# Optimization experiments

Measured on AMD Instinct MI355X. Metric: run time of the kernel, lower is better.

## Reference

```python
import jax, jax.numpy as jnp
import numpy as np

ALIGN_CORNERS = True
APPLY_SMOOTHSTEP = True

SIZES = [(32, 32, 32), (64, 64, 64), (128, 128, 128), (256, 256, 256)]
FEAT_DIMS = [4, 4, 4, 4]
N_POINTS = 1048576  # 2**20 sample points (e.g. 8192 rays x 128 samples)


def setup_inputs() -> dict:
    key = jax.random.key(0)
    ks = jax.random.split(key, 1 + len(SIZES))
    # grid_sample-style coords in [-1, 1], layout [1, 1, 1, N, 3] (x, y, z)
    grid = jax.random.uniform(ks[0], (1, 1, 1, N_POINTS, 3), dtype=jnp.float32) * 2.0 - 1.0
    inp = {"grid": grid}
    for i, (size, c) in enumerate(zip(SIZES, FEAT_DIMS)):
        # original init: (rand(1,C,1,1,1)*2-1).repeat over spatial; use randn volumes for a
        # non-degenerate baseline (same shapes/math path)
        inp[f"vol{i}"] = jax.random.normal(ks[1 + i], (1, c, *size), dtype=jnp.float32)
    return inp


def _smooth_sample(vol, grid_pts):
    """Trilinear sample with border padding, align_corners=True, smoothstep weights.

    vol: [C, D, H, W]; grid_pts: [P, 3] with (x, y, z) in [-1, 1].
    Returns [C, P].
    """
    C, D, H, W = vol.shape
    # unnormalize (align_corners=True): [-1,1] -> [0, dim-1]; border padding via clip
    x = jnp.clip((grid_pts[:, 0] + 1.0) * 0.5 * (W - 1), 0.0, W - 1)
    y = jnp.clip((grid_pts[:, 1] + 1.0) * 0.5 * (H - 1), 0.0, H - 1)
    z = jnp.clip((grid_pts[:, 2] + 1.0) * 0.5 * (D - 1), 0.0, D - 1)

    x0 = jnp.floor(x); y0 = jnp.floor(y); z0 = jnp.floor(z)
    tx = x - x0; ty = y - y0; tz = z - z0
    if APPLY_SMOOTHSTEP:
        tx = tx * tx * (3.0 - 2.0 * tx)
        ty = ty * ty * (3.0 - 2.0 * ty)
        tz = tz * tz * (3.0 - 2.0 * tz)

    x0i = x0.astype(jnp.int32); x1i = jnp.minimum(x0i + 1, W - 1)
    y0i = y0.astype(jnp.int32); y1i = jnp.minimum(y0i + 1, H - 1)
    z0i = z0.astype(jnp.int32); z1i = jnp.minimum(z0i + 1, D - 1)

    # 8 corner gathers -> [C, P]
    c000 = vol[:, z0i, y0i, x0i]; c001 = vol[:, z0i, y0i, x1i]
    c010 = vol[:, z0i, y1i, x0i]; c011 = vol[:, z0i, y1i, x1i]
    c100 = vol[:, z1i, y0i, x0i]; c101 = vol[:, z1i, y0i, x1i]
    c110 = vol[:, z1i, y1i, x0i]; c111 = vol[:, z1i, y1i, x1i]

    c00 = c000 + (c001 - c000) * tx
    c01 = c010 + (c011 - c010) * tx
    c10 = c100 + (c101 - c100) * tx
    c11 = c110 + (c111 - c110) * tx
    c0 = c00 + (c01 - c00) * ty
    c1 = c10 + (c11 - c10) * ty
    return c0 + (c1 - c0) * tz


def reference(grid, vol0, vol1, vol2, vol3):
    # grid: [1, 1, 1, N, 3] -> [N, 3]
    pts = grid.reshape(-1, 3)
    n = pts.shape[0]
    out = []
    for vol in (vol0, vol1, vol2, vol3):
        feat = _smooth_sample(vol[0], pts)            # [C, N]
        out.append(feat.reshape(1, -1, 1, 1, n))      # grid_sample output layout
    return jnp.concatenate(out, axis=1)               # [1, sum(C), 1, 1, N]
```

## Files before the change

### kernel.cpp

```cpp
#include <hip/hip_runtime.h>

#define NPTS 1048576
#define NB 32
#define NBINS (NB * NB * NB)

typedef float v4f __attribute__((ext_vector_type(4)));

__device__ __forceinline__ void nt_store4(const float4& f, float4* p) {
    __builtin_nontemporal_store(*(const v4f*)&f, (v4f*)p);
}


__device__ __forceinline__ float4 lerp4(const float4 a, const float4 b, const float t) {
    return make_float4(a.x + (b.x - a.x) * t,
                       a.y + (b.y - a.y) * t,
                       a.z + (b.z - a.z) * t,
                       a.w + (b.w - a.w) * t);
}

struct CoordW { float tx, ty, tz; int b00, b01, b10, b11, x0, x1; };

template<int D>
__device__ __forceinline__ CoordW mkcoord(float gx, float gy, float gz) {
    CoordW c;
    float x = fminf(fmaxf((gx + 1.0f) * (0.5f * (float)(D - 1)), 0.0f), (float)(D - 1));
    float y = fminf(fmaxf((gy + 1.0f) * (0.5f * (float)(D - 1)), 0.0f), (float)(D - 1));
    float z = fminf(fmaxf((gz + 1.0f) * (0.5f * (float)(D - 1)), 0.0f), (float)(D - 1));
    float xf = floorf(x), yf = floorf(y), zf = floorf(z);
    float tx = x - xf, ty = y - yf, tz = z - zf;
    c.tx = tx * tx * (3.0f - 2.0f * tx);
    c.ty = ty * ty * (3.0f - 2.0f * ty);
    c.tz = tz * tz * (3.0f - 2.0f * tz);
    int x0 = (int)xf, y0 = (int)yf, z0 = (int)zf;
    int y1 = min(y0 + 1, D - 1), z1 = min(z0 + 1, D - 1);
    c.x0 = x0;
    c.x1 = min(x0 + 1, D - 1);
    c.b00 = (z0 * D + y0) * D;
    c.b01 = (z0 * D + y1) * D;
    c.b10 = (z1 * D + y0) * D;
    c.b11 = (z1 * D + y1) * D;
    return c;
}

__device__ __forceinline__ float4 reduce8(const float4* q, const CoordW& c) {
    float4 c00 = lerp4(q[0], q[1], c.tx);
    float4 c01 = lerp4(q[2], q[3], c.tx);
    float4 c10 = lerp4(q[4], q[5], c.tx);
    float4 c11 = lerp4(q[6], q[7], c.tx);
    float4 c0 = lerp4(c00, c01, c.ty);
    float4 c1 = lerp4(c10, c11, c.ty);
    return lerp4(c0, c1, c.tz);
}


#define DHW0 (32 * 32 * 32)
#define DHW1 (64 * 64 * 64)
#define DHW2 (128 * 128 * 128)

__global__ __launch_bounds__(256) void xpose_all_kernel(
    const float* __restrict__ v0, const float* __restrict__ v1, const float* __restrict__ v2,
    float4* __restrict__ w0, float4* __restrict__ w1, float4* __restrict__ w2)
{
    constexpr int B2 = DHW2 / 256, B1 = DHW1 / 256;
    int b = blockIdx.x;
    int t = threadIdx.x;
    if (b < B2) {
        int v = b * 256 + t;
        w2[v] = make_float4(v2[v], v2[v + DHW2], v2[v + 2 * DHW2], v2[v + 3 * DHW2]);
    } else if (b < B2 + B1) {
        int v = (b - B2) * 256 + t;
        w1[v] = make_float4(v1[v], v1[v + DHW1], v1[v + 2 * DHW1], v1[v + 3 * DHW1]);
    } else {
        int v = (b - B2 - B1) * 256 + t;
        w0[v] = make_float4(v0[v], v0[v + DHW0], v0[v + 2 * DHW0], v0[v + 3 * DHW0]);
    }
}


__device__ __forceinline__ int bin_of(float gx, float gy, float gz) {
    float ux = fminf(fmaxf((gx + 1.0f) * 0.5f, 0.0f), 1.0f);
    float uy = fminf(fmaxf((gy + 1.0f) * 0.5f, 0.0f), 1.0f);
    float uz = fminf(fmaxf((gz + 1.0f) * 0.5f, 0.0f), 1.0f);
    int bx = min((int)(ux * (float)NB), NB - 1);
    int by = min((int)(uy * (float)NB), NB - 1);
    int bz = min((int)(uz * (float)NB), NB - 1);
    return (bz * NB + by) * NB + bx;
}

__global__ __launch_bounds__(256) void bin_hist_kernel(const float* __restrict__ grid,
                                                       unsigned* __restrict__ hist) {
    int p = blockIdx.x * blockDim.x + threadIdx.x;
    float gx = grid[3 * p + 0];
    float gy = grid[3 * p + 1];
    float gz = grid[3 * p + 2];
    atomicAdd(&hist[bin_of(gx, gy, gz)], 1u);
}

__global__ __launch_bounds__(1024) void scan_kernel(const unsigned* __restrict__ hist,
                                                    unsigned* __restrict__ offsets) {
    __shared__ unsigned partial[1024];
    const int t = threadIdx.x;
    const int base = t * 32;
    unsigned sum = 0;
#pragma unroll
    for (int i = 0; i < 32; ++i) sum += hist[base + i];
    partial[t] = sum;
    __syncthreads();
    for (int off = 1; off < 1024; off <<= 1) {
        unsigned v = (t >= off) ? partial[t - off] : 0u;
        __syncthreads();
        partial[t] += v;
        __syncthreads();
    }
    unsigned run = partial[t] - sum;
#pragma unroll
    for (int i = 0; i < 32; ++i) {
        offsets[base + i] = run;
        run += hist[base + i];
    }
}

__global__ __launch_bounds__(256) void scatter_kernel(const float* __restrict__ grid,
                                                      unsigned* __restrict__ offsets,
                                                      float4* __restrict__ sorted,
                                                      int* __restrict__ inv) {
    int p = blockIdx.x * blockDim.x + threadIdx.x;
    float gx = grid[3 * p + 0];
    float gy = grid[3 * p + 1];
    float gz = grid[3 * p + 2];
    int b = bin_of(gx, gy, gz);
    unsigned pos = atomicAdd(&offsets[b], 1u);
    sorted[pos] = make_float4(gx, gy, gz, __int_as_float(p));
    inv[p] = (int)pos;
}


__global__ __launch_bounds__(256, 4) void gather_sorted_kernel(
    const float4* __restrict__ sorted,
    const float4* __restrict__ w0, const float4* __restrict__ w1,
    const float4* __restrict__ w2, const float* __restrict__ v3,
    float4* __restrict__ wsout)
{
    int bid = blockIdx.x;
    int sb = (bid & 7) * (int)(gridDim.x >> 3) + (bid >> 3);
    int s = sb * 256 + (int)threadIdx.x;
    float4 gp = sorted[s];
    float gx = gp.x, gy = gp.y, gz = gp.z;

    CoordW c0 = mkcoord<32>(gx, gy, gz);
    CoordW c1 = mkcoord<64>(gx, gy, gz);
    CoordW c2 = mkcoord<128>(gx, gy, gz);
    CoordW c3 = mkcoord<256>(gx, gy, gz);

    float4 qa[8], qb[8], qc[8];
    qa[0] = w0[c0.b00 + c0.x0]; qa[1] = w0[c0.b00 + c0.x1];
    qa[2] = w0[c0.b01 + c0.x0]; qa[3] = w0[c0.b01 + c0.x1];
    qa[4] = w0[c0.b10 + c0.x0]; qa[5] = w0[c0.b10 + c0.x1];
    qa[6] = w0[c0.b11 + c0.x0]; qa[7] = w0[c0.b11 + c0.x1];

    qb[0] = w1[c1.b00 + c1.x0]; qb[1] = w1[c1.b00 + c1.x1];
    qb[2] = w1[c1.b01 + c1.x0]; qb[3] = w1[c1.b01 + c1.x1];
    qb[4] = w1[c1.b10 + c1.x0]; qb[5] = w1[c1.b10 + c1.x1];
    qb[6] = w1[c1.b11 + c1.x0]; qb[7] = w1[c1.b11 + c1.x1];

    qc[0] = w2[c2.b00 + c2.x0]; qc[1] = w2[c2.b00 + c2.x1];
    qc[2] = w2[c2.b01 + c2.x0]; qc[3] = w2[c2.b01 + c2.x1];
    qc[4] = w2[c2.b10 + c2.x0]; qc[5] = w2[c2.b10 + c2.x1];
    qc[6] = w2[c2.b11 + c2.x0]; qc[7] = w2[c2.b11 + c2.x1];

    const int xm = min(c3.x0, 254);
    const bool edge = (c3.x0 == 255);
    float2 qd[16];
#pragma unroll
    for (int ch = 0; ch < 4; ++ch) {
        const float* __restrict__ vc = v3 + (size_t)ch * (256 * 256 * 256);
        qd[ch * 4 + 0] = *(const float2*)(vc + c3.b00 + xm);
        qd[ch * 4 + 1] = *(const float2*)(vc + c3.b01 + xm);
        qd[ch * 4 + 2] = *(const float2*)(vc + c3.b10 + xm);
        qd[ch * 4 + 3] = *(const float2*)(vc + c3.b11 + xm);
    }

    float4 f0 = reduce8(qa, c0);
    float4 f1 = reduce8(qb, c1);
    float4 f2 = reduce8(qc, c2);

    float r3[4];
#pragma unroll
    for (int ch = 0; ch < 4; ++ch) {
        float v00a = edge ? qd[ch * 4 + 0].y : qd[ch * 4 + 0].x, v00b = qd[ch * 4 + 0].y;
        float v01a = edge ? qd[ch * 4 + 1].y : qd[ch * 4 + 1].x, v01b = qd[ch * 4 + 1].y;
        float v10a = edge ? qd[ch * 4 + 2].y : qd[ch * 4 + 2].x, v10b = qd[ch * 4 + 2].y;
        float v11a = edge ? qd[ch * 4 + 3].y : qd[ch * 4 + 3].x, v11b = qd[ch * 4 + 3].y;
        float c00 = v00a + (v00b - v00a) * c3.tx;
        float c01 = v01a + (v01b - v01a) * c3.tx;
        float c10 = v10a + (v10b - v10a) * c3.tx;
        float c11 = v11a + (v11b - v11a) * c3.tx;
        float e0 = c00 + (c01 - c00) * c3.ty;
        float e1 = c10 + (c11 - c10) * c3.ty;
        r3[ch] = e0 + (e1 - e0) * c3.tz;
    }
    float4 f3 = make_float4(r3[0], r3[1], r3[2], r3[3]);

    float4* w = wsout + (size_t)s * 4;
    nt_store4(f0, w + 0);
    nt_store4(f1, w + 1);
    nt_store4(f2, w + 2);
    nt_store4(f3, w + 3);
}


__device__ __forceinline__ void permute_one(const float4* __restrict__ wsout,
                                            const int* __restrict__ inv,
                                            float* __restrict__ out, int p) {
    int s = inv[p];
    const float4* w = wsout + (size_t)s * 4;
    float4 f0 = w[0], f1 = w[1], f2 = w[2], f3 = w[3];
    __builtin_nontemporal_store(f0.x, &out[ 0 * NPTS + p]);
    __builtin_nontemporal_store(f0.y, &out[ 1 * NPTS + p]);
    __builtin_nontemporal_store(f0.z, &out[ 2 * NPTS + p]);
    __builtin_nontemporal_store(f0.w, &out[ 3 * NPTS + p]);
    __builtin_nontemporal_store(f1.x, &out[ 4 * NPTS + p]);
    __builtin_nontemporal_store(f1.y, &out[ 5 * NPTS + p]);
    __builtin_nontemporal_store(f1.z, &out[ 6 * NPTS + p]);
    __builtin_nontemporal_store(f1.w, &out[ 7 * NPTS + p]);
    __builtin_nontemporal_store(f2.x, &out[ 8 * NPTS + p]);
    __builtin_nontemporal_store(f2.y, &out[ 9 * NPTS + p]);
    __builtin_nontemporal_store(f2.z, &out[10 * NPTS + p]);
    __builtin_nontemporal_store(f2.w, &out[11 * NPTS + p]);
    __builtin_nontemporal_store(f3.x, &out[12 * NPTS + p]);
    __builtin_nontemporal_store(f3.y, &out[13 * NPTS + p]);
    __builtin_nontemporal_store(f3.z, &out[14 * NPTS + p]);
    __builtin_nontemporal_store(f3.w, &out[15 * NPTS + p]);
}

__global__ __launch_bounds__(256) void permute_kernel(const float4* __restrict__ wsout,
                                                      const int* __restrict__ inv,
                                                      float* __restrict__ out) {
    int p = blockIdx.x * blockDim.x + threadIdx.x;
    permute_one(wsout, inv, out, p);
    permute_one(wsout, inv, out, p + NPTS / 2);
}


template<int D>
__device__ __forceinline__ float4 sample_inter(const float4* __restrict__ v,
                                               float gx, float gy, float gz) {
    CoordW c = mkcoord<D>(gx, gy, gz);
    float4 q[8];
    q[0] = v[c.b00 + c.x0]; q[1] = v[c.b00 + c.x1];
    q[2] = v[c.b01 + c.x0]; q[3] = v[c.b01 + c.x1];
    q[4] = v[c.b10 + c.x0]; q[5] = v[c.b10 + c.x1];
    q[6] = v[c.b11 + c.x0]; q[7] = v[c.b11 + c.x1];
    return reduce8(q, c);
}

template<int D>
__device__ __forceinline__ float4 sample_direct(const float* __restrict__ v,
                                                float gx, float gy, float gz) {
    CoordW c = mkcoord<D>(gx, gy, gz);
    float r[4];
#pragma unroll
    for (int ch = 0; ch < 4; ++ch) {
        const float* __restrict__ vc = v + (size_t)ch * (D * D * D);
        float c000 = vc[c.b00 + c.x0], c001 = vc[c.b00 + c.x1];
        float c010 = vc[c.b01 + c.x0], c011 = vc[c.b01 + c.x1];
        float c100 = vc[c.b10 + c.x0], c101 = vc[c.b10 + c.x1];
        float c110 = vc[c.b11 + c.x0], c111 = vc[c.b11 + c.x1];
        float c00 = c000 + (c001 - c000) * c.tx;
        float c01 = c010 + (c011 - c010) * c.tx;
        float c10 = c100 + (c101 - c100) * c.tx;
        float c11 = c110 + (c111 - c110) * c.tx;
        float e0 = c00 + (c01 - c00) * c.ty;
        float e1 = c10 + (c11 - c10) * c.ty;
        r[ch] = e0 + (e1 - e0) * c.tz;
    }
    return make_float4(r[0], r[1], r[2], r[3]);
}

__global__ __launch_bounds__(256) void mg_direct_kernel(
    const float* __restrict__ grid,
    const float* __restrict__ v0, const float* __restrict__ v1,
    const float* __restrict__ v2, const float* __restrict__ v3,
    float* __restrict__ out)
{
    int p = blockIdx.x * blockDim.x + threadIdx.x;
    float gx = grid[3 * p + 0];
    float gy = grid[3 * p + 1];
    float gz = grid[3 * p + 2];
    float4 f0 = sample_direct<32>(v0, gx, gy, gz);
    float4 f1 = sample_direct<64>(v1, gx, gy, gz);
    float4 f2 = sample_direct<128>(v2, gx, gy, gz);
    float4 f3 = sample_direct<256>(v3, gx, gy, gz);
    out[ 0 * NPTS + p] = f0.x; out[ 1 * NPTS + p] = f0.y;
    out[ 2 * NPTS + p] = f0.z; out[ 3 * NPTS + p] = f0.w;
    out[ 4 * NPTS + p] = f1.x; out[ 5 * NPTS + p] = f1.y;
    out[ 6 * NPTS + p] = f1.z; out[ 7 * NPTS + p] = f1.w;
    out[ 8 * NPTS + p] = f2.x; out[ 9 * NPTS + p] = f2.y;
    out[10 * NPTS + p] = f2.z; out[11 * NPTS + p] = f2.w;
    out[12 * NPTS + p] = f3.x; out[13 * NPTS + p] = f3.y;
    out[14 * NPTS + p] = f3.z; out[15 * NPTS + p] = f3.w;
}

__global__ __launch_bounds__(256) void mg_inter_kernel(
    const float* __restrict__ grid,
    const float4* __restrict__ w0, const float4* __restrict__ w1,
    const float4* __restrict__ w2, const float* __restrict__ v3,
    float* __restrict__ out)
{
    int p = blockIdx.x * blockDim.x + threadIdx.x;
    float gx = grid[3 * p + 0];
    float gy = grid[3 * p + 1];
    float gz = grid[3 * p + 2];
    float4 f0 = sample_inter<32>(w0, gx, gy, gz);
    float4 f1 = sample_inter<64>(w1, gx, gy, gz);
    float4 f2 = sample_inter<128>(w2, gx, gy, gz);
    float4 f3 = sample_direct<256>(v3, gx, gy, gz);
    out[ 0 * NPTS + p] = f0.x; out[ 1 * NPTS + p] = f0.y;
    out[ 2 * NPTS + p] = f0.z; out[ 3 * NPTS + p] = f0.w;
    out[ 4 * NPTS + p] = f1.x; out[ 5 * NPTS + p] = f1.y;
    out[ 6 * NPTS + p] = f1.z; out[ 7 * NPTS + p] = f1.w;
    out[ 8 * NPTS + p] = f2.x; out[ 9 * NPTS + p] = f2.y;
    out[10 * NPTS + p] = f2.z; out[11 * NPTS + p] = f2.w;
    out[12 * NPTS + p] = f3.x; out[13 * NPTS + p] = f3.y;
    out[14 * NPTS + p] = f3.z; out[15 * NPTS + p] = f3.w;
}


extern "C" void kernel_launch(void* const* d_in, const int* in_sizes, int n_in,
                              void* d_out, int out_size, void* d_ws, size_t ws_size,
                              hipStream_t stream) {
    const float* grid = (const float*)d_in[0];
    const float* v0   = (const float*)d_in[1];
    const float* v1   = (const float*)d_in[2];
    const float* v2   = (const float*)d_in[3];
    const float* v3   = (const float*)d_in[4];
    float* out = (float*)d_out;

    constexpr size_t OFF_WSOUT  = 0;
    constexpr size_t OFF_SORTED = OFF_WSOUT  + (size_t)NPTS * 64;
    constexpr size_t OFF_W2     = OFF_SORTED + (size_t)NPTS * 16;
    constexpr size_t OFF_W1     = OFF_W2     + (size_t)DHW2 * 16;
    constexpr size_t OFF_W0     = OFF_W1     + (size_t)DHW1 * 16;
    constexpr size_t OFF_INV    = OFF_W0     + (size_t)DHW0 * 16;
    constexpr size_t OFF_HIST   = OFF_INV    + (size_t)NPTS * 4;
    constexpr size_t OFF_OFFS   = OFF_HIST   + (size_t)NBINS * 4;
    constexpr size_t WS_FULL    = OFF_OFFS   + (size_t)NBINS * 4;
    constexpr size_t WS_INTER   = (size_t)(DHW0 + DHW1 + DHW2) * 16;

    const int threads = 256;
    const int pt_blocks = NPTS / threads;
    char* ws = (char*)d_ws;

    if (ws_size >= WS_FULL) {
        float4*   wsout  = (float4*)(ws + OFF_WSOUT);
        float4*   sorted = (float4*)(ws + OFF_SORTED);
        float4*   w2     = (float4*)(ws + OFF_W2);
        float4*   w1     = (float4*)(ws + OFF_W1);
        float4*   w0     = (float4*)(ws + OFF_W0);
        int*      inv    = (int*)   (ws + OFF_INV);
        unsigned* hist   = (unsigned*)(ws + OFF_HIST);
        unsigned* offs   = (unsigned*)(ws + OFF_OFFS);

        (void)hipMemsetAsync(hist, 0, (size_t)NBINS * 4, stream);
        xpose_all_kernel<<<(DHW0 + DHW1 + DHW2) / threads, threads, 0, stream>>>(
            v0, v1, v2, w0, w1, w2);
        bin_hist_kernel<<<pt_blocks, threads, 0, stream>>>(grid, hist);
        scan_kernel<<<1, 1024, 0, stream>>>(hist, offs);
        scatter_kernel<<<pt_blocks, threads, 0, stream>>>(grid, offs, sorted, inv);
        gather_sorted_kernel<<<pt_blocks, threads, 0, stream>>>(sorted, w0, w1, w2, v3, wsout);
        permute_kernel<<<pt_blocks / 2, threads, 0, stream>>>(wsout, inv, out);
    } else if (ws_size >= WS_INTER) {
        float4* w0 = (float4*)d_ws;
        float4* w1 = w0 + DHW0;
        float4* w2 = w1 + DHW1;
        xpose_all_kernel<<<(DHW0 + DHW1 + DHW2) / threads, threads, 0, stream>>>(
            v0, v1, v2, w0, w1, w2);
        mg_inter_kernel<<<pt_blocks, threads, 0, stream>>>(grid, w0, w1, w2, v3, out);
    } else {
        mg_direct_kernel<<<pt_blocks, threads, 0, stream>>>(grid, v0, v1, v2, v3, out);
    }
}
```

Measured before the change: 660.4 us.

## Store volumes and intermediates as bf16 with paired-x layout, scatter by point index

Converts all four volumes, including the 256^3 one, into a bf16 channel-interleaved layout where each 16-byte load holds an x-adjacent pair of 4-channel voxels. Each trilinear sample then needs 4 loads instead of 8. The gather kernel writes bf16-packed results directly at the original point index, which removes the inverse-permutation array and the indirect permute pass. The final kernel only unpacks and stores. This reduces gather and intermediate bandwidth but rounds both the volume values and the outputs to bf16, a precision loss that may break tolerance. The conversion pass over the 256 MB v3 also adds traffic on every call.

```diff
diff --git a/kernel.cpp b/kernel.cpp
--- a/kernel.cpp
+++ b/kernel.cpp
@@ -4,11 +4,41 @@
 #define NB 32
 #define NBINS (NB * NB * NB)
 
+#define D0c 32
+#define D1c 64
+#define D2c 128
+#define D3c 256
+#define VOX0 (D0c * D0c * D0c)
+#define VOX1 (D1c * D1c * D1c)
+#define VOX2 (D2c * D2c * D2c)
+#define VOX3 (D3c * D3c * D3c)
+
 typedef float v4f __attribute__((ext_vector_type(4)));
-
-__device__ __forceinline__ void nt_store4(const float4& f, float4* p) {
+typedef unsigned uv4 __attribute__((ext_vector_type(4)));
+
+__device__ __forceinline__ void nt_store4f(const float4& f, float4* p) {
     __builtin_nontemporal_store(*(const v4f*)&f, (v4f*)p);
 }
+__device__ __forceinline__ void nt_store4u(const uint4& u, uint4* p) {
+    __builtin_nontemporal_store(*(const uv4*)&u, (uv4*)p);
+}
+
+__device__ __forceinline__ uint4 load16(const void* p) {
+    uint4 r;
+    __builtin_memcpy(&r, p, sizeof(uint4));
+    return r;
+}
+
+
+__device__ __forceinline__ unsigned bf1(float a) {
+    unsigned u = __float_as_uint(a);
+    return (u + 0x7FFFu + ((u >> 16) & 1u)) >> 16;
+}
+__device__ __forceinline__ unsigned bfpack(float lo, float hi) {
+    return bf1(lo) | (bf1(hi) << 16);
+}
+__device__ __forceinline__ float bflo(unsigned u) { return __uint_as_float(u << 16); }
+__device__ __forceinline__ float bfhi(unsigned u) { return __uint_as_float(u & 0xFFFF0000u); }
 
 
 __device__ __forceinline__ float4 lerp4(const float4 a, const float4 b, const float t) {
@@ -42,6 +72,26 @@
     return c;
 }
 
+__device__ __forceinline__ float4 rowlerp(const uint4 q, const bool edge, const float tx) {
+    float b0 = bflo(q.z), b1 = bfhi(q.z), b2 = bflo(q.w), b3 = bfhi(q.w);
+    float a0 = edge ? b0 : bflo(q.x);
+    float a1 = edge ? b1 : bfhi(q.x);
+    float a2 = edge ? b2 : bflo(q.y);
+    float a3 = edge ? b3 : bfhi(q.y);
+    return make_float4(a0 + (b0 - a0) * tx, a1 + (b1 - a1) * tx,
+                       a2 + (b2 - a2) * tx, a3 + (b3 - a3) * tx);
+}
+
+__device__ __forceinline__ float4 reduce_bf(const uint4 q[4], const CoordW& c, bool edge) {
+    float4 r00 = rowlerp(q[0], edge, c.tx);
+    float4 r01 = rowlerp(q[1], edge, c.tx);
+    float4 r10 = rowlerp(q[2], edge, c.tx);
+    float4 r11 = rowlerp(q[3], edge, c.tx);
+    float4 e0 = lerp4(r00, r01, c.ty);
+    float4 e1 = lerp4(r10, r11, c.ty);
+    return lerp4(e0, e1, c.tz);
+}
+
 __device__ __forceinline__ float4 reduce8(const float4* q, const CoordW& c) {
     float4 c00 = lerp4(q[0], q[1], c.tx);
     float4 c01 = lerp4(q[2], q[3], c.tx);
@@ -53,27 +103,45 @@
 }
 
 
-#define DHW0 (32 * 32 * 32)
-#define DHW1 (64 * 64 * 64)
-#define DHW2 (128 * 128 * 128)
-
-__global__ __launch_bounds__(256) void xpose_all_kernel(
+template<int VOX>
+__device__ __forceinline__ void conv_pair(const float* __restrict__ v,
+                                          uint4* __restrict__ w, int i) {
+    const float2* __restrict__ c0 = (const float2*)(v);
+    const float2* __restrict__ c1 = (const float2*)(v + VOX);
+    const float2* __restrict__ c2 = (const float2*)(v + 2 * VOX);
+    const float2* __restrict__ c3 = (const float2*)(v + 3 * VOX);
+    float2 a = c0[i], b = c1[i], c = c2[i], d = c3[i];
+    uint4 u;
+    u.x = bfpack(a.x, b.x);
+    u.y = bfpack(c.x, d.x);
+    u.z = bfpack(a.y, b.y);
+    u.w = bfpack(c.y, d.y);
+    nt_store4u(u, &w[i]);
+}
+
+__global__ __launch_bounds__(256) void conv_all_kernel(
+    const float* __restrict__ v0, const float* __restrict__ v1,
+    const float* __restrict__ v2, const float* __restrict__ v3,
+    uint4* __restrict__ w0, uint4* __restrict__ w1,
+    uint4* __restrict__ w2, uint4* __restrict__ w3)
+{
+    constexpr int P3 = VOX3 / 512, P2 = VOX2 / 512, P1 = VOX1 / 512;
+    int b = blockIdx.x, t = threadIdx.x;
+    if (b < P3)                 conv_pair<VOX3>(v3, w3, b * 256 + t);
+    else if (b < P3 + P2)       conv_pair<VOX2>(v2, w2, (b - P3) * 256 + t);
+    else if (b < P3 + P2 + P1)  conv_pair<VOX1>(v1, w1, (b - P3 - P2) * 256 + t);
+    else                        conv_pair<VOX0>(v0, w0, (b - P3 - P2 - P1) * 256 + t);
+}
+
+__global__ __launch_bounds__(256) void conv_small_kernel(
     const float* __restrict__ v0, const float* __restrict__ v1, const float* __restrict__ v2,
-    float4* __restrict__ w0, float4* __restrict__ w1, float4* __restrict__ w2)
-{
-    constexpr int B2 = DHW2 / 256, B1 = DHW1 / 256;
-    int b = blockIdx.x;
-    int t = threadIdx.x;
-    if (b < B2) {
-        int v = b * 256 + t;
-        w2[v] = make_float4(v2[v], v2[v + DHW2], v2[v + 2 * DHW2], v2[v + 3 * DHW2]);
-    } else if (b < B2 + B1) {
-        int v = (b - B2) * 256 + t;
-        w1[v] = make_float4(v1[v], v1[v + DHW1], v1[v + 2 * DHW1], v1[v + 3 * DHW1]);
-    } else {
-        int v = (b - B2 - B1) * 256 + t;
-        w0[v] = make_float4(v0[v], v0[v + DHW0], v0[v + 2 * DHW0], v0[v + 3 * DHW0]);
-    }
+    uint4* __restrict__ w0, uint4* __restrict__ w1, uint4* __restrict__ w2)
+{
+    constexpr int P2 = VOX2 / 512, P1 = VOX1 / 512;
+    int b = blockIdx.x, t = threadIdx.x;
+    if (b < P2)            conv_pair<VOX2>(v2, w2, b * 256 + t);
+    else if (b < P2 + P1)  conv_pair<VOX1>(v1, w1, (b - P2) * 256 + t);
+    else                   conv_pair<VOX0>(v0, w0, (b - P2 - P1) * 256 + t);
 }
 
 
@@ -122,8 +190,7 @@
 
 __global__ __launch_bounds__(256) void scatter_kernel(const float* __restrict__ grid,
                                                       unsigned* __restrict__ offsets,
-                                                      float4* __restrict__ sorted,
-                                                      int* __restrict__ inv) {
+                                                      float4* __restrict__ sorted) {
     int p = blockIdx.x * blockDim.x + threadIdx.x;
     float gx = grid[3 * p + 0];
     float gy = grid[3 * p + 1];
@@ -131,114 +198,152 @@
     int b = bin_of(gx, gy, gz);
     unsigned pos = atomicAdd(&offsets[b], 1u);
     sorted[pos] = make_float4(gx, gy, gz, __int_as_float(p));
-    inv[p] = (int)pos;
-}
-
-
-__global__ __launch_bounds__(256, 4) void gather_sorted_kernel(
+}
+
+
+template<int D>
+__device__ __forceinline__ void fetch_rows(const char* __restrict__ w, const CoordW& c,
+                                           int xm, uint4 q[4]) {
+    q[0] = load16(w + 8 * (c.b00 + xm));
+    q[1] = load16(w + 8 * (c.b01 + xm));
+    q[2] = load16(w + 8 * (c.b10 + xm));
+    q[3] = load16(w + 8 * (c.b11 + xm));
+}
+
+__global__ __launch_bounds__(256) void gather_a_kernel(
     const float4* __restrict__ sorted,
-    const float4* __restrict__ w0, const float4* __restrict__ w1,
-    const float4* __restrict__ w2, const float* __restrict__ v3,
-    float4* __restrict__ wsout)
+    const char* __restrict__ w0, const char* __restrict__ w1,
+    const char* __restrict__ w2, const char* __restrict__ w3,
+    uint4* __restrict__ wsout)
 {
     int bid = blockIdx.x;
     int sb = (bid & 7) * (int)(gridDim.x >> 3) + (bid >> 3);
     int s = sb * 256 + (int)threadIdx.x;
     float4 gp = sorted[s];
     float gx = gp.x, gy = gp.y, gz = gp.z;
+    int p = __float_as_int(gp.w);
 
     CoordW c0 = mkcoord<32>(gx, gy, gz);
     CoordW c1 = mkcoord<64>(gx, gy, gz);
     CoordW c2 = mkcoord<128>(gx, gy, gz);
     CoordW c3 = mkcoord<256>(gx, gy, gz);
-
-    float4 qa[8], qb[8], qc[8];
-    qa[0] = w0[c0.b00 + c0.x0]; qa[1] = w0[c0.b00 + c0.x1];
-    qa[2] = w0[c0.b01 + c0.x0]; qa[3] = w0[c0.b01 + c0.x1];
-    qa[4] = w0[c0.b10 + c0.x0]; qa[5] = w0[c0.b10 + c0.x1];
-    qa[6] = w0[c0.b11 + c0.x0]; qa[7] = w0[c0.b11 + c0.x1];
-
-    qb[0] = w1[c1.b00 + c1.x0]; qb[1] = w1[c1.b00 + c1.x1];
-    qb[2] = w1[c1.b01 + c1.x0]; qb[3] = w1[c1.b01 + c1.x1];
-    qb[4] = w1[c1.b10 + c1.x0]; qb[5] = w1[c1.b10 + c1.x1];
-    qb[6] = w1[c1.b11 + c1.x0]; qb[7] = w1[c1.b11 + c1.x1];
-
-    qc[0] = w2[c2.b00 + c2.x0]; qc[1] = w2[c2.b00 + c2.x1];
-    qc[2] = w2[c2.b01 + c2.x0]; qc[3] = w2[c2.b01 + c2.x1];
-    qc[4] = w2[c2.b10 + c2.x0]; qc[5] = w2[c2.b10 + c2.x1];
-    qc[6] = w2[c2.b11 + c2.x0]; qc[7] = w2[c2.b11 + c2.x1];
-
-    const int xm = min(c3.x0, 254);
-    const bool edge = (c3.x0 == 255);
+    int xm0 = min(c0.x0, 30);  bool e0 = (c0.x0 == 31);
+    int xm1 = min(c1.x0, 62);  bool e1 = (c1.x0 == 63);
+    int xm2 = min(c2.x0, 126); bool e2 = (c2.x0 == 127);
+    int xm3 = min(c3.x0, 254); bool e3 = (c3.x0 == 255);
+
+    uint4 qa[4], qb[4], qc[4], qd[4];
+    fetch_rows<32>(w0, c0, xm0, qa);
+    fetch_rows<64>(w1, c1, xm1, qb);
+    fetch_rows<128>(w2, c2, xm2, qc);
+    fetch_rows<256>(w3, c3, xm3, qd);
+
+    float4 f0 = reduce_bf(qa, c0, e0);
+    float4 f1 = reduce_bf(qb, c1, e1);
+    float4 f2 = reduce_bf(qc, c2, e2);
+    float4 f3 = reduce_bf(qd, c3, e3);
+
+    uint4 ua, ub;
+    ua.x = bfpack(f0.x, f0.y); ua.y = bfpack(f0.z, f0.w);
+    ua.z = bfpack(f1.x, f1.y); ua.w = bfpack(f1.z, f1.w);
+    ub.x = bfpack(f2.x, f2.y); ub.y = bfpack(f2.z, f2.w);
+    ub.z = bfpack(f3.x, f3.y); ub.w = bfpack(f3.z, f3.w);
+
+    uint4* w = wsout + (size_t)p * 2;
+    nt_store4u(ua, w + 0);
+    nt_store4u(ub, w + 1);
+}
+
+
+__global__ __launch_bounds__(256) void gather_b_kernel(
+    const float4* __restrict__ sorted,
+    const char* __restrict__ w0, const char* __restrict__ w1,
+    const char* __restrict__ w2, const float* __restrict__ v3,
+    uint4* __restrict__ wsout)
+{
+    int bid = blockIdx.x;
+    int sb = (bid & 7) * (int)(gridDim.x >> 3) + (bid >> 3);
+    int s = sb * 256 + (int)threadIdx.x;
+    float4 gp = sorted[s];
+    float gx = gp.x, gy = gp.y, gz = gp.z;
+    int p = __float_as_int(gp.w);
+
+    CoordW c0 = mkcoord<32>(gx, gy, gz);
+    CoordW c1 = mkcoord<64>(gx, gy, gz);
+    CoordW c2 = mkcoord<128>(gx, gy, gz);
+    CoordW c3 = mkcoord<256>(gx, gy, gz);
+    int xm0 = min(c0.x0, 30);  bool e0 = (c0.x0 == 31);
+    int xm1 = min(c1.x0, 62);  bool e1 = (c1.x0 == 63);
+    int xm2 = min(c2.x0, 126); bool e2 = (c2.x0 == 127);
+    int xm3 = min(c3.x0, 254); bool e3 = (c3.x0 == 255);
+
+    uint4 qa[4], qb[4], qc[4];
+    fetch_rows<32>(w0, c0, xm0, qa);
+    fetch_rows<64>(w1, c1, xm1, qb);
+    fetch_rows<128>(w2, c2, xm2, qc);
+
     float2 qd[16];
 #pragma unroll
     for (int ch = 0; ch < 4; ++ch) {
-        const float* __restrict__ vc = v3 + (size_t)ch * (256 * 256 * 256);
-        qd[ch * 4 + 0] = *(const float2*)(vc + c3.b00 + xm);
-        qd[ch * 4 + 1] = *(const float2*)(vc + c3.b01 + xm);
-        qd[ch * 4 + 2] = *(const float2*)(vc + c3.b10 + xm);
-        qd[ch * 4 + 3] = *(const float2*)(vc + c3.b11 + xm);
-    }
-
-    float4 f0 = reduce8(qa, c0);
-    float4 f1 = reduce8(qb, c1);
-    float4 f2 = reduce8(qc, c2);
+        const float* __restrict__ vc = v3 + (size_t)ch * VOX3;
+        qd[ch * 4 + 0] = *(const float2*)(vc + c3.b00 + xm3);
+        qd[ch * 4 + 1] = *(const float2*)(vc + c3.b01 + xm3);
+        qd[ch * 4 + 2] = *(const float2*)(vc + c3.b10 + xm3);
+        qd[ch * 4 + 3] = *(const float2*)(vc + c3.b11 + xm3);
+    }
+
+    float4 f0 = reduce_bf(qa, c0, e0);
+    float4 f1 = reduce_bf(qb, c1, e1);
+    float4 f2 = reduce_bf(qc, c2, e2);
 
     float r3[4];
 #pragma unroll
     for (int ch = 0; ch < 4; ++ch) {
-        float v00a = edge ? qd[ch * 4 + 0].y : qd[ch * 4 + 0].x, v00b = qd[ch * 4 + 0].y;
-        float v01a = edge ? qd[ch * 4 + 1].y : qd[ch * 4 + 1].x, v01b = qd[ch * 4 + 1].y;
-        float v10a = edge ? qd[ch * 4 + 2].y : qd[ch * 4 + 2].x, v10b = qd[ch * 4 + 2].y;
-        float v11a = edge ? qd[ch * 4 + 3].y : qd[ch * 4 + 3].x, v11b = qd[ch * 4 + 3].y;
+        float v00a = e3 ? qd[ch * 4 + 0].y : qd[ch * 4 + 0].x, v00b = qd[ch * 4 + 0].y;
+        float v01a = e3 ? qd[ch * 4 + 1].y : qd[ch * 4 + 1].x, v01b = qd[ch * 4 + 1].y;
+        float v10a = e3 ? qd[ch * 4 + 2].y : qd[ch * 4 + 2].x, v10b = qd[ch * 4 + 2].y;
+        float v11a = e3 ? qd[ch * 4 + 3].y : qd[ch * 4 + 3].x, v11b = qd[ch * 4 + 3].y;
         float c00 = v00a + (v00b - v00a) * c3.tx;
         float c01 = v01a + (v01b - v01a) * c3.tx;
         float c10 = v10a + (v10b - v10a) * c3.tx;
         float c11 = v11a + (v11b - v11a) * c3.tx;
-        float e0 = c00 + (c01 - c00) * c3.ty;
-        float e1 = c10 + (c11 - c10) * c3.ty;
-        r3[ch] = e0 + (e1 - e0) * c3.tz;
-    }
-    float4 f3 = make_float4(r3[0], r3[1], r3[2], r3[3]);
-
-    float4* w = wsout + (size_t)s * 4;
-    nt_store4(f0, w + 0);
-    nt_store4(f1, w + 1);
-    nt_store4(f2, w + 2);
-    nt_store4(f3, w + 3);
-}
-
-
-__device__ __forceinline__ void permute_one(const float4* __restrict__ wsout,
-                                            const int* __restrict__ inv,
-                                            float* __restrict__ out, int p) {
-    int s = inv[p];
-    const float4* w = wsout + (size_t)s * 4;
-    float4 f0 = w[0], f1 = w[1], f2 = w[2], f3 = w[3];
-    __builtin_nontemporal_store(f0.x, &out[ 0 * NPTS + p]);
-    __builtin_nontemporal_store(f0.y, &out[ 1 * NPTS + p]);
-    __builtin_nontemporal_store(f0.z, &out[ 2 * NPTS + p]);
-    __builtin_nontemporal_store(f0.w, &out[ 3 * NPTS + p]);
-    __builtin_nontemporal_store(f1.x, &out[ 4 * NPTS + p]);
-    __builtin_nontemporal_store(f1.y, &out[ 5 * NPTS + p]);
-    __builtin_nontemporal_store(f1.z, &out[ 6 * NPTS + p]);
-    __builtin_nontemporal_store(f1.w, &out[ 7 * NPTS + p]);
-    __builtin_nontemporal_store(f2.x, &out[ 8 * NPTS + p]);
-    __builtin_nontemporal_store(f2.y, &out[ 9 * NPTS + p]);
-    __builtin_nontemporal_store(f2.z, &out[10 * NPTS + p]);
-    __builtin_nontemporal_store(f2.w, &out[11 * NPTS + p]);
-    __builtin_nontemporal_store(f3.x, &out[12 * NPTS + p]);
-    __builtin_nontemporal_store(f3.y, &out[13 * NPTS + p]);
-    __builtin_nontemporal_store(f3.z, &out[14 * NPTS + p]);
-    __builtin_nontemporal_store(f3.w, &out[15 * NPTS + p]);
-}
-
-__global__ __launch_bounds__(256) void permute_kernel(const float4* __restrict__ wsout,
-                                                      const int* __restrict__ inv,
-                                                      float* __restrict__ out) {
+        float ee0 = c00 + (c01 - c00) * c3.ty;
+        float ee1 = c10 + (c11 - c10) * c3.ty;
+        r3[ch] = ee0 + (ee1 - ee0) * c3.tz;
+    }
+
+    uint4 ua, ub;
+    ua.x = bfpack(f0.x, f0.y); ua.y = bfpack(f0.z, f0.w);
+    ua.z = bfpack(f1.x, f1.y); ua.w = bfpack(f1.z, f1.w);
+    ub.x = bfpack(f2.x, f2.y); ub.y = bfpack(f2.z, f2.w);
+    ub.z = bfpack(r3[0], r3[1]); ub.w = bfpack(r3[2], r3[3]);
+
+    uint4* w = wsout + (size_t)p * 2;
+    nt_store4u(ua, w + 0);
+    nt_store4u(ub, w + 1);
+}
+
+
+__global__ __launch_bounds__(256) void final_kernel(const uint4* __restrict__ wsout,
+                                                    float* __restrict__ out) {
     int p = blockIdx.x * blockDim.x + threadIdx.x;
-    permute_one(wsout, inv, out, p);
-    permute_one(wsout, inv, out, p + NPTS / 2);
+    uint4 a = wsout[2 * p], b = wsout[2 * p + 1];
+    __builtin_nontemporal_store(bflo(a.x), &out[ 0 * NPTS + p]);
+    __builtin_nontemporal_store(bfhi(a.x), &out[ 1 * NPTS + p]);
+    __builtin_nontemporal_store(bflo(a.y), &out[ 2 * NPTS + p]);
+    __builtin_nontemporal_store(bfhi(a.y), &out[ 3 * NPTS + p]);
+    __builtin_nontemporal_store(bflo(a.z), &out[ 4 * NPTS + p]);
+    __builtin_nontemporal_store(bfhi(a.z), &out[ 5 * NPTS + p]);
+    __builtin_nontemporal_store(bflo(a.w), &out[ 6 * NPTS + p]);
+    __builtin_nontemporal_store(bfhi(a.w), &out[ 7 * NPTS + p]);
+    __builtin_nontemporal_store(bflo(b.x), &out[ 8 * NPTS + p]);
+    __builtin_nontemporal_store(bfhi(b.x), &out[ 9 * NPTS + p]);
+    __builtin_nontemporal_store(bflo(b.y), &out[10 * NPTS + p]);
+    __builtin_nontemporal_store(bfhi(b.y), &out[11 * NPTS + p]);
+    __builtin_nontemporal_store(bflo(b.z), &out[12 * NPTS + p]);
+    __builtin_nontemporal_store(bfhi(b.z), &out[13 * NPTS + p]);
+    __builtin_nontemporal_store(bflo(b.w), &out[14 * NPTS + p]);
+    __builtin_nontemporal_store(bfhi(b.w), &out[15 * NPTS + p]);
 }
 
 
@@ -277,6 +382,49 @@
     return make_float4(r[0], r[1], r[2], r[3]);
 }
 
+__global__ __launch_bounds__(256) void xpose_all_kernel(
+    const float* __restrict__ v0, const float* __restrict__ v1, const float* __restrict__ v2,
+    float4* __restrict__ w0, float4* __restrict__ w1, float4* __restrict__ w2)
+{
+    constexpr int B2 = VOX2 / 256, B1 = VOX1 / 256;
+    int b = blockIdx.x;
+    int t = threadIdx.x;
+    if (b < B2) {
+        int v = b * 256 + t;
+        w2[v] = make_float4(v2[v], v2[v + VOX2], v2[v + 2 * VOX2], v2[v + 3 * VOX2]);
+    } else if (b < B2 + B1) {
+        int v = (b - B2) * 256 + t;
+        w1[v] = make_float4(v1[v], v1[v + VOX1], v1[v + 2 * VOX1], v1[v + 3 * VOX1]);
+    } else {
+        int v = (b - B2 - B1) * 256 + t;
+        w0[v] = make_float4(v0[v], v0[v + VOX0], v0[v + 2 * VOX0], v0[v + 3 * VOX0]);
+    }
+}
+
+__global__ __launch_bounds__(256) void mg_inter_kernel(
+    const float* __restrict__ grid,
+    const float4* __restrict__ w0, const float4* __restrict__ w1,
+    const float4* __restrict__ w2, const float* __restrict__ v3,
+    float* __restrict__ out)
+{
+    int p = blockIdx.x * blockDim.x + threadIdx.x;
+    float gx = grid[3 * p + 0];
+    float gy = grid[3 * p + 1];
+    float gz = grid[3 * p + 2];
+    float4 f0 = sample_inter<32>(w0, gx, gy, gz);
+    float4 f1 = sample_inter<64>(w1, gx, gy, gz);
+    float4 f2 = sample_inter<128>(w2, gx, gy, gz);
+    float4 f3 = sample_direct<256>(v3, gx, gy, gz);
+    out[ 0 * NPTS + p] = f0.x; out[ 1 * NPTS + p] = f0.y;
+    out[ 2 * NPTS + p] = f0.z; out[ 3 * NPTS + p] = f0.w;
+    out[ 4 * NPTS + p] = f1.x; out[ 5 * NPTS + p] = f1.y;
+    out[ 6 * NPTS + p] = f1.z; out[ 7 * NPTS + p] = f1.w;
+    out[ 8 * NPTS + p] = f2.x; out[ 9 * NPTS + p] = f2.y;
+    out[10 * NPTS + p] = f2.z; out[11 * NPTS + p] = f2.w;
+    out[12 * NPTS + p] = f3.x; out[13 * NPTS + p] = f3.y;
+    out[14 * NPTS + p] = f3.z; out[15 * NPTS + p] = f3.w;
+}
+
 __global__ __launch_bounds__(256) void mg_direct_kernel(
     const float* __restrict__ grid,
     const float* __restrict__ v0, const float* __restrict__ v1,
@@ -301,30 +449,6 @@
     out[14 * NPTS + p] = f3.z; out[15 * NPTS + p] = f3.w;
 }
 
-__global__ __launch_bounds__(256) void mg_inter_kernel(
-    const float* __restrict__ grid,
-    const float4* __restrict__ w0, const float4* __restrict__ w1,
-    const float4* __restrict__ w2, const float* __restrict__ v3,
-    float* __restrict__ out)
-{
-    int p = blockIdx.x * blockDim.x + threadIdx.x;
-    float gx = grid[3 * p + 0];
-    float gy = grid[3 * p + 1];
-    float gz = grid[3 * p + 2];
-    float4 f0 = sample_inter<32>(w0, gx, gy, gz);
-    float4 f1 = sample_inter<64>(w1, gx, gy, gz);
-    float4 f2 = sample_inter<128>(w2, gx, gy, gz);
-    float4 f3 = sample_direct<256>(v3, gx, gy, gz);
-    out[ 0 * NPTS + p] = f0.x; out[ 1 * NPTS + p] = f0.y;
-    out[ 2 * NPTS + p] = f0.z; out[ 3 * NPTS + p] = f0.w;
-    out[ 4 * NPTS + p] = f1.x; out[ 5 * NPTS + p] = f1.y;
-    out[ 6 * NPTS + p] = f1.z; out[ 7 * NPTS + p] = f1.w;
-    out[ 8 * NPTS + p] = f2.x; out[ 9 * NPTS + p] = f2.y;
-    out[10 * NPTS + p] = f2.z; out[11 * NPTS + p] = f2.w;
-    out[12 * NPTS + p] = f3.x; out[13 * NPTS + p] = f3.y;
-    out[14 * NPTS + p] = f3.z; out[15 * NPTS + p] = f3.w;
-}
-
 
 extern "C" void kernel_launch(void* const* d_in, const int* in_sizes, int n_in,
                               void* d_out, int out_size, void* d_ws, size_t ws_size,
@@ -336,44 +460,62 @@
     const float* v3   = (const float*)d_in[4];
     float* out = (float*)d_out;
 
-    constexpr size_t OFF_WSOUT  = 0;
-    constexpr size_t OFF_SORTED = OFF_WSOUT  + (size_t)NPTS * 64;
-    constexpr size_t OFF_W2     = OFF_SORTED + (size_t)NPTS * 16;
-    constexpr size_t OFF_W1     = OFF_W2     + (size_t)DHW2 * 16;
-    constexpr size_t OFF_W0     = OFF_W1     + (size_t)DHW1 * 16;
-    constexpr size_t OFF_INV    = OFF_W0     + (size_t)DHW0 * 16;
-    constexpr size_t OFF_HIST   = OFF_INV    + (size_t)NPTS * 4;
-    constexpr size_t OFF_OFFS   = OFF_HIST   + (size_t)NBINS * 4;
-    constexpr size_t WS_FULL    = OFF_OFFS   + (size_t)NBINS * 4;
-    constexpr size_t WS_INTER   = (size_t)(DHW0 + DHW1 + DHW2) * 16;
+    constexpr size_t SZ_W3   = (size_t)VOX3 * 8;
+    constexpr size_t SZ_W2   = (size_t)VOX2 * 8;
+    constexpr size_t SZ_W1   = (size_t)VOX1 * 8;
+    constexpr size_t SZ_W0   = (size_t)VOX0 * 8;
+    constexpr size_t SZ_SORT = (size_t)NPTS * 16;
+    constexpr size_t SZ_WSO  = (size_t)NPTS * 32;
+    constexpr size_t SZ_H    = (size_t)NBINS * 4;
+
+    constexpr size_t WS_A = SZ_W3 + SZ_W2 + SZ_W1 + SZ_W0 + SZ_SORT + SZ_WSO + 2 * SZ_H;
+    constexpr size_t WS_B = WS_A - SZ_W3;
+    constexpr size_t WS_INTER = (size_t)(VOX0 + VOX1 + VOX2) * 16;
 
     const int threads = 256;
     const int pt_blocks = NPTS / threads;
     char* ws = (char*)d_ws;
 
-    if (ws_size >= WS_FULL) {
-        float4*   wsout  = (float4*)(ws + OFF_WSOUT);
-        float4*   sorted = (float4*)(ws + OFF_SORTED);
-        float4*   w2     = (float4*)(ws + OFF_W2);
-        float4*   w1     = (float4*)(ws + OFF_W1);
-        float4*   w0     = (float4*)(ws + OFF_W0);
-        int*      inv    = (int*)   (ws + OFF_INV);
-        unsigned* hist   = (unsigned*)(ws + OFF_HIST);
-        unsigned* offs   = (unsigned*)(ws + OFF_OFFS);
-
-        (void)hipMemsetAsync(hist, 0, (size_t)NBINS * 4, stream);
-        xpose_all_kernel<<<(DHW0 + DHW1 + DHW2) / threads, threads, 0, stream>>>(
-            v0, v1, v2, w0, w1, w2);
+    if (ws_size >= WS_A) {
+        char*     w3     = ws;
+        char*     w2     = w3 + SZ_W3;
+        char*     w1     = w2 + SZ_W2;
+        char*     w0     = w1 + SZ_W1;
+        float4*   sorted = (float4*)(w0 + SZ_W0);
+        uint4*    wsout  = (uint4*)((char*)sorted + SZ_SORT);
+        unsigned* hist   = (unsigned*)((char*)wsout + SZ_WSO);
+        unsigned* offs   = (unsigned*)((char*)hist + SZ_H);
+
+        (void)hipMemsetAsync(hist, 0, SZ_H, stream);
+        conv_all_kernel<<<(VOX0 + VOX1 + VOX2 + VOX3) / 512, threads, 0, stream>>>(
+            v0, v1, v2, v3, (uint4*)w0, (uint4*)w1, (uint4*)w2, (uint4*)w3);
         bin_hist_kernel<<<pt_blocks, threads, 0, stream>>>(grid, hist);
         scan_kernel<<<1, 1024, 0, stream>>>(hist, offs);
-        scatter_kernel<<<pt_blocks, threads, 0, stream>>>(grid, offs, sorted, inv);
-        gather_sorted_kernel<<<pt_blocks, threads, 0, stream>>>(sorted, w0, w1, w2, v3, wsout);
-        permute_kernel<<<pt_blocks / 2, threads, 0, stream>>>(wsout, inv, out);
+        scatter_kernel<<<pt_blocks, threads, 0, stream>>>(grid, offs, sorted);
+        gather_a_kernel<<<pt_blocks, threads, 0, stream>>>(sorted, w0, w1, w2, w3, wsout);
+        final_kernel<<<pt_blocks, threads, 0, stream>>>(wsout, out);
+    } else if (ws_size >= WS_B) {
+        char*     w2     = ws;
+        char*     w1     = w2 + SZ_W2;
+        char*     w0     = w1 + SZ_W1;
+        float4*   sorted = (float4*)(w0 + SZ_W0);
+        uint4*    wsout  = (uint4*)((char*)sorted + SZ_SORT);
+        unsigned* hist   = (unsigned*)((char*)wsout + SZ_WSO);
+        unsigned* offs   = (unsigned*)((char*)hist + SZ_H);
+
+        (void)hipMemsetAsync(hist, 0, SZ_H, stream);
+        conv_small_kernel<<<(VOX0 + VOX1 + VOX2) / 512, threads, 0, stream>>>(
+            v0, v1, v2, (uint4*)w0, (uint4*)w1, (uint4*)w2);
+        bin_hist_kernel<<<pt_blocks, threads, 0, stream>>>(grid, hist);
+        scan_kernel<<<1, 1024, 0, stream>>>(hist, offs);
+        scatter_kernel<<<pt_blocks, threads, 0, stream>>>(grid, offs, sorted);
+        gather_b_kernel<<<pt_blocks, threads, 0, stream>>>(sorted, w0, w1, w2, v3, wsout);
+        final_kernel<<<pt_blocks, threads, 0, stream>>>(wsout, out);
     } else if (ws_size >= WS_INTER) {
         float4* w0 = (float4*)d_ws;
-        float4* w1 = w0 + DHW0;
-        float4* w2 = w1 + DHW1;
-        xpose_all_kernel<<<(DHW0 + DHW1 + DHW2) / threads, threads, 0, stream>>>(
+        float4* w1 = w0 + VOX0;
+        float4* w2 = w1 + VOX1;
+        xpose_all_kernel<<<(VOX0 + VOX1 + VOX2) / threads, threads, 0, stream>>>(
             v0, v1, v2, w0, w1, w2);
         mg_inter_kernel<<<pt_blocks, threads, 0, stream>>>(grid, w0, w1, w2, v3, out);
     } else {
```

New measurement: 669.7 us. No clear change (+1.4%).
